# Performance work log

Hardware: AMD Instinct MI355X
Metric: run time of the kernel (lower is better)

## Reference

```python
import jax, jax.numpy as jnp
import numpy as np

HEADS = 16
DIM_HEAD = 64

def setup_inputs() -> dict:
    key = jax.random.key(0)
    ks = jax.random.split(key, 7)
    B, Nq, Dq = 4, 2048, 1024
    Nk, Dc = 1024, 768
    inner = HEADS * DIM_HEAD  # 1024
    sq = 1.0 / np.sqrt(Dq)
    sc = 1.0 / np.sqrt(Dc)
    si = 1.0 / np.sqrt(inner)
    return {
        "x": jax.random.normal(ks[0], (B, Nq, Dq), dtype=jnp.float32),
        "context": jax.random.normal(ks[1], (B, Nk, Dc), dtype=jnp.float32),
        "Wq": jax.random.normal(ks[2], (Dq, inner), dtype=jnp.float32) * sq,
        "Wk": jax.random.normal(ks[3], (Dc, inner), dtype=jnp.float32) * sc,
        "Wv": jax.random.normal(ks[4], (Dc, inner), dtype=jnp.float32) * sc,
        "Wo": jax.random.normal(ks[5], (inner, Dq), dtype=jnp.float32) * si,
        "bo": jax.random.normal(ks[6], (Dq,), dtype=jnp.float32) * 0.01,
    }

def reference(x, context, Wq, Wk, Wv, Wo, bo):
    B, Nq, _ = x.shape
    Nk = context.shape[1]
    h, dh = HEADS, DIM_HEAD
    # projections (no bias on q/k/v, matching nn.Linear(bias=False))
    q = (x @ Wq).reshape(B, Nq, h, dh)        # [B,Nq,h,dh]
    k = (context @ Wk).reshape(B, Nk, h, dh)  # [B,Nk,h,dh]
    v = (context @ Wv).reshape(B, Nk, h, dh)
    scale = 1.0 / jnp.sqrt(jnp.asarray(dh, dtype=x.dtype))
    # scores: [B,h,Nq,Nk]
    scores = jnp.einsum('bqhd,bkhd->bhqk', q, k) * scale
    attn = jax.nn.softmax(scores, axis=-1)
    out = jnp.einsum('bhqk,bkhd->bqhd', attn, v).reshape(B, Nq, h * dh)
    return out @ Wo + bo
```

## Files before the change

kernel.cpp:

```cpp
#include <hip/hip_runtime.h>

typedef __bf16 bf16;
typedef __bf16 bf16x2 __attribute__((ext_vector_type(2)));
typedef __bf16 bf16x4 __attribute__((ext_vector_type(4)));
typedef __bf16 bf16x8 __attribute__((ext_vector_type(8)));
typedef float f32x4 __attribute__((ext_vector_type(4)));

#define MFMA(a, b, c) __builtin_amdgcn_mfma_f32_16x16x32_bf16(a, b, c, 0, 0, 0)

#define GLD16(gptr, ldsptr)                                                        \
  __builtin_amdgcn_global_load_lds(                                                \
      (const __attribute__((address_space(1))) unsigned int*)(gptr),               \
      (__attribute__((address_space(3))) unsigned int*)(ldsptr), 16, 0, 0)

union I4B8 { int4 i; bf16x8 v; };
union HI { bf16x2 h; int i; };

__global__ __launch_bounds__(256) void prep_k(const float* __restrict__ x, bf16* __restrict__ xb,
                                              const float* __restrict__ ctx, bf16* __restrict__ ctxb,
                                              const float* __restrict__ Wq, bf16* __restrict__ WqT,
                                              const float* __restrict__ Wk, bf16* __restrict__ WkvT,
                                              const float* __restrict__ Wv,
                                              const float* __restrict__ Wo, bf16* __restrict__ WoT) {
  __shared__ float t[32][33];
  const int bid = blockIdx.x;
  if (bid < 5632) {
    const float* in; bf16* out; size_t i;
    if (bid < 4096) { in = x; out = xb; i = ((size_t)bid * 256 + threadIdx.x) * 8; }
    else { in = ctx; out = ctxb; i = ((size_t)(bid - 4096) * 256 + threadIdx.x) * 8; }
    const float4 a = *(const float4*)(in + i);
    const float4 b = *(const float4*)(in + i + 4);
    bf16x8 o;
    o[0] = (bf16)a.x; o[1] = (bf16)a.y; o[2] = (bf16)a.z; o[3] = (bf16)a.w;
    o[4] = (bf16)b.x; o[5] = (bf16)b.y; o[6] = (bf16)b.z; o[7] = (bf16)b.w;
    *(bf16x8*)(out + i) = o;
    return;
  }
  const int tt = bid - 5632;
  const int z = tt >> 10, rem = tt & 1023;
  const float* in; bf16* out; int R; float sc = 1.0f;
  if (z == 0)      { in = Wq; out = WqT;                R = 1024; sc = 0.18033688f; }
  else if (z == 1) { in = Wk; out = WkvT;               R = 768; }
  else if (z == 2) { in = Wv; out = WkvT + 1024 * 768;  R = 768; }
  else             { in = Wo; out = WoT;                R = 1024; }
  const int c0 = (rem & 31) * 32, r0 = (rem >> 5) * 32;
  if (r0 >= R) return;
  const int tx = threadIdx.x & 31, ty = threadIdx.x >> 5;
#pragma unroll
  for (int i = 0; i < 4; i++)
    t[ty + i * 8][tx] = in[(size_t)(r0 + ty + i * 8) * 1024 + c0 + tx];
  __syncthreads();
#pragma unroll
  for (int i = 0; i < 4; i++)
    out[(size_t)(c0 + ty + i * 8) * R + r0 + tx] = (bf16)(t[tx][ty + i * 8] * sc);
}

template <int MODE>
__device__ __forceinline__ void gemm_body(const bf16* __restrict__ A,
                                          const bf16* __restrict__ Bt,
                                          int K, int m0, int n0,
                                          void* __restrict__ C0,
                                          const float* __restrict__ bias,
                                          bf16* As, bf16* Bs) {
  const int tid = threadIdx.x;
  const int lane = tid & 63, wave = tid >> 6;
  const int wm = wave >> 1, wn = wave & 1;
  const int q = lane >> 4, c = lane & 15;

  f32x4 acc[4][4] = {};
  const int r = tid >> 3;
  const int col8 = ((tid & 7) * 8) ^ ((r & 7) * 8);
  const bf16* Ag = A + (size_t)(m0 + r) * K + col8;
  const bf16* Bg = Bt + (size_t)(n0 + r) * K + col8;
  const size_t K32 = (size_t)K * 32;
  bf16* AsW = As + wave * 512;
  bf16* BsW = Bs + wave * 512;
  const int swz = (c & 7) * 8;

  for (int k0 = 0; k0 < K; k0 += 64) {
    __syncthreads();
    GLD16(Ag + k0,            AsW);
    GLD16(Ag + k0 + K32,      AsW + 2048);
    GLD16(Ag + k0 + 2 * K32,  AsW + 4096);
    GLD16(Ag + k0 + 3 * K32,  AsW + 6144);
    GLD16(Bg + k0,            BsW);
    GLD16(Bg + k0 + K32,      BsW + 2048);
    GLD16(Bg + k0 + 2 * K32,  BsW + 4096);
    GLD16(Bg + k0 + 3 * K32,  BsW + 6144);
    __syncthreads();
#pragma unroll
    for (int kk = 0; kk < 2; kk++) {
      const int cx = (kk * 32 + q * 8) ^ swz;
      bf16x8 af[4], bfr[4];
#pragma unroll
      for (int mi = 0; mi < 4; mi++)
        af[mi] = *(const bf16x8*)&As[(wm * 64 + mi * 16 + c) * 64 + cx];
#pragma unroll
      for (int ni = 0; ni < 4; ni++)
        bfr[ni] = *(const bf16x8*)&Bs[(wn * 64 + ni * 16 + c) * 64 + cx];
      __builtin_amdgcn_s_setprio(1);
#pragma unroll
      for (int mi = 0; mi < 4; mi++)
#pragma unroll
        for (int ni = 0; ni < 4; ni++) {
          if constexpr (MODE == 2)
            acc[mi][ni] = MFMA(af[mi], bfr[ni], acc[mi][ni]);
          else
            acc[mi][ni] = MFMA(bfr[ni], af[mi], acc[mi][ni]);
        }
      __builtin_amdgcn_s_setprio(0);
    }
  }

  if constexpr (MODE == 0 || MODE == 1) {
#pragma unroll
    for (int ni = 0; ni < 4; ni++) {
      const int col = n0 + wn * 64 + ni * 16 + q * 4;
      float4 bv4 = {};
      if constexpr (MODE == 1) bv4 = *(const float4*)&bias[col];
#pragma unroll
      for (int mi = 0; mi < 4; mi++) {
        const int row = m0 + wm * 64 + mi * 16 + c;
        if constexpr (MODE == 0) {
          bf16x4 vv;
#pragma unroll
          for (int r2 = 0; r2 < 4; r2++) vv[r2] = (bf16)acc[mi][ni][r2];
          *(bf16x4*)&((bf16*)C0)[(size_t)row * 1024 + col] = vv;
        } else {
          f32x4 vv;
          vv[0] = acc[mi][ni][0] + bv4.x; vv[1] = acc[mi][ni][1] + bv4.y;
          vv[2] = acc[mi][ni][2] + bv4.z; vv[3] = acc[mi][ni][3] + bv4.w;
          *(f32x4*)&((float*)C0)[(size_t)row * 1024 + col] = vv;
        }
      }
    }
  } else {
#pragma unroll
    for (int ni = 0; ni < 4; ni++) {
      const int col = n0 + wn * 64 + ni * 16 + c;
#pragma unroll
      for (int mi = 0; mi < 4; mi++) {
        const int rbase = m0 + wm * 64 + mi * 16 + q * 4;
        const int b = rbase >> 10, key = rbase & 1023;
        bf16* VT = (bf16*)C0;
        const int h = col >> 6, d = col & 63;
        const int kl = key & 63;
        const int pkey = (key & ~63) | (kl & 32) | ((kl & 12) << 1) | ((kl & 16) >> 2);
        bf16x4 vv;
#pragma unroll
        for (int r2 = 0; r2 < 4; r2++) vv[r2] = (bf16)acc[mi][ni][r2];
        *(bf16x4*)&VT[((size_t)(b * 16 + h) * 64 + d) * 1024 + pkey] = vv;
      }
    }
  }
}

__global__ __launch_bounds__(256) void proj_k(const bf16* __restrict__ xb,
                                              const bf16* __restrict__ ctxb,
                                              const bf16* __restrict__ WqT,
                                              const bf16* __restrict__ WkvT,
                                              bf16* __restrict__ Q,
                                              bf16* __restrict__ Kp,
                                              bf16* __restrict__ VT) {
  __shared__ __align__(16) bf16 As[8192];
  __shared__ __align__(16) bf16 Bs[8192];
  const int bid = blockIdx.x;
  if (bid < 512) {
    const int s = (bid & 7) * 64 + (bid >> 3);
    gemm_body<0>(xb, WqT, 1024, (s >> 3) * 128, (s & 7) * 128, Q, nullptr, As, Bs);
  } else if (bid < 768) {
    const int t = bid - 512;
    const int s = (t & 7) * 32 + (t >> 3);
    gemm_body<0>(ctxb, WkvT, 768, (s >> 3) * 128, (s & 7) * 128, Kp, nullptr, As, Bs);
  } else {
    const int t = bid - 768;
    const int s = (t & 7) * 32 + (t >> 3);
    gemm_body<2>(ctxb, WkvT + (size_t)1024 * 768, 768, (s >> 3) * 128, (s & 7) * 128,
                 VT, nullptr, As, Bs);
  }
}

__global__ __launch_bounds__(256) void out_k(const bf16* __restrict__ O,
                                             const bf16* __restrict__ WoT,
                                             float* __restrict__ out,
                                             const float* __restrict__ bo) {
  __shared__ __align__(16) bf16 As[8192];
  __shared__ __align__(16) bf16 Bs[8192];
  const int bid = blockIdx.x;
  const int s = (bid & 7) * 64 + (bid >> 3);
  gemm_body<1>(O, WoT, 1024, (s >> 3) * 128, (s & 7) * 128, out, bo, As, Bs);
}

__global__ __launch_bounds__(256, 2) void attn_k(const bf16* __restrict__ Qg,
                                                 const bf16* __restrict__ Kg,
                                                 const bf16* __restrict__ VTg,
                                                 bf16* __restrict__ Og) {
  __shared__ __align__(16) bf16 Ks[64][72];
  __shared__ __align__(16) bf16 Vt[64][72];
  const int tid = threadIdx.x;
  const int lane = tid & 63, w = tid >> 6;
  const int q = lane >> 4, c = lane & 15;
  const int bid = blockIdx.x;
  const int pair = (bid & 7) * 8 + (bid >> 6);
  const int head = pair & 15, b = pair >> 4;
  const int q0 = ((bid >> 3) & 7) * 256;

  bf16x8 aQ[4][2];
#pragma unroll
  for (int mj = 0; mj < 4; mj++)
#pragma unroll
    for (int ks = 0; ks < 2; ks++)
      aQ[mj][ks] = *(const bf16x8*)(Qg + (size_t)(b * 2048 + q0 + w * 64 + mj * 16 + c) * 1024 +
                                    head * 64 + ks * 32 + q * 8);

  f32x4 o[4][4] = {};
  f32x4 ol[4] = {};
  bf16x8 vone;
#pragma unroll
  for (int i = 0; i < 8; i++) vone[i] = (bf16)1.0f;

  const int srow = tid >> 2, sc = tid & 3;
  const bf16* Kbase = Kg + (size_t)(b * 1024 + srow) * 1024 + head * 64 + sc * 16;
  const bf16* Vbase = VTg + ((size_t)(b * 16 + head) * 64 + srow) * 1024 + sc * 16;

  bf16x8 rk0 = *(const bf16x8*)(Kbase);
  bf16x8 rk1 = *(const bf16x8*)(Kbase + 8);
  bf16x8 rv0 = *(const bf16x8*)(Vbase);
  bf16x8 rv1 = *(const bf16x8*)(Vbase + 8);

  for (int kt = 0; kt < 16; kt++) {
    __syncthreads();
    *(bf16x8*)&Ks[srow][sc * 16]     = rk0;
    *(bf16x8*)&Ks[srow][sc * 16 + 8] = rk1;
    *(bf16x8*)&Vt[srow][sc * 16]     = rv0;
    *(bf16x8*)&Vt[srow][sc * 16 + 8] = rv1;
    if (kt < 15) {
      const size_t ko = (size_t)(kt + 1) * 64 * 1024;
      const int vo = (kt + 1) * 64;
      rk0 = *(const bf16x8*)(Kbase + ko);
      rk1 = *(const bf16x8*)(Kbase + ko + 8);
      rv0 = *(const bf16x8*)(Vbase + vo);
      rv1 = *(const bf16x8*)(Vbase + vo + 8);
    }
    __syncthreads();

    f32x4 st[4][4] = {};
#pragma unroll
    for (int ks = 0; ks < 2; ks++) {
      bf16x8 ak[4];
#pragma unroll
      for (int ni = 0; ni < 4; ni++) ak[ni] = *(const bf16x8*)&Ks[ni * 16 + c][ks * 32 + q * 8];
      __builtin_amdgcn_s_setprio(1);
#pragma unroll
      for (int mj = 0; mj < 4; mj++)
#pragma unroll
        for (int ni = 0; ni < 4; ni++)
          st[mj][ni] = MFMA(ak[ni], aQ[mj][ks], st[mj][ni]);
      __builtin_amdgcn_s_setprio(0);
    }

    int pk[4][4][2];
#pragma unroll
    for (int mj = 0; mj < 4; mj++)
#pragma unroll
      for (int ni = 0; ni < 4; ni++) {
        float p0 = __builtin_amdgcn_exp2f(st[mj][ni][0]);
        float p1 = __builtin_amdgcn_exp2f(st[mj][ni][1]);
        float p2 = __builtin_amdgcn_exp2f(st[mj][ni][2]);
        float p3 = __builtin_amdgcn_exp2f(st[mj][ni][3]);
        HI h0, h1;
        h0.h[0] = (bf16)p0; h0.h[1] = (bf16)p1;
        h1.h[0] = (bf16)p2; h1.h[1] = (bf16)p3;
        pk[mj][ni][0] = h0.i;
        pk[mj][ni][1] = h1.i;
      }

#pragma unroll
    for (int ks2 = 0; ks2 < 2; ks2++) {
      bf16x8 bv[4];
#pragma unroll
      for (int ni = 0; ni < 4; ni++)
        bv[ni] = *(const bf16x8*)&Vt[ni * 16 + c][ks2 * 32 + q * 8];
#pragma unroll
      for (int mi = 0; mi < 4; mi++) {
        I4B8 pa;
        pa.i.x = pk[mi][2 * ks2][0];
        pa.i.y = pk[mi][2 * ks2][1];
        pa.i.z = pk[mi][2 * ks2 + 1][0];
        pa.i.w = pk[mi][2 * ks2 + 1][1];
        __builtin_amdgcn_s_setprio(1);
#pragma unroll
        for (int ni = 0; ni < 4; ni++)
          o[mi][ni] = MFMA(pa.v, bv[ni], o[mi][ni]);
        ol[mi] = MFMA(pa.v, vone, ol[mi]);
        __builtin_amdgcn_s_setprio(0);
      }
    }
  }

#pragma unroll
  for (int mi = 0; mi < 4; mi++) {
    float inv[4];
#pragma unroll
    for (int r = 0; r < 4; r++) inv[r] = 1.0f / ol[mi][r];
#pragma unroll
    for (int ni = 0; ni < 4; ni++)
#pragma unroll
      for (int r = 0; r < 4; r++) {
        const int qrow = q0 + w * 64 + mi * 16 + q * 4 + r;
        const int col = head * 64 + ni * 16 + c;
        Og[(size_t)(b * 2048 + qrow) * 1024 + col] = (bf16)(o[mi][ni][r] * inv[r]);
      }
  }
}

extern "C" void kernel_launch(void* const* d_in, const int* in_sizes, int n_in,
                              void* d_out, int out_size, void* d_ws, size_t ws_size,
                              hipStream_t stream) {
  (void)in_sizes; (void)n_in; (void)out_size; (void)ws_size;
  const float* x   = (const float*)d_in[0];
  const float* ctx = (const float*)d_in[1];
  const float* Wq  = (const float*)d_in[2];
  const float* Wk  = (const float*)d_in[3];
  const float* Wv  = (const float*)d_in[4];
  const float* Wo  = (const float*)d_in[5];
  const float* bo  = (const float*)d_in[6];
  float* out = (float*)d_out;

  char* ws = (char*)d_ws;
  const size_t MB = 1u << 20;
  bf16* WqT  = (bf16*)(ws);
  bf16* WkvT = (bf16*)(ws + 2 * MB);
  bf16* WoT  = (bf16*)(ws + 5 * MB);
  bf16* ctxb = (bf16*)(ws + 7 * MB);
  bf16* xb   = (bf16*)(ws + 13 * MB);
  bf16* Q    = (bf16*)(ws + 29 * MB);
  bf16* Kp   = (bf16*)(ws + 45 * MB);
  bf16* VT   = (bf16*)(ws + 53 * MB);
  bf16* O    = xb;

  prep_k<<<5632 + 4096, 256, 0, stream>>>(x, xb, ctx, ctxb, Wq, WqT, Wk, WkvT, Wv, Wo, WoT);

  proj_k<<<1024, 256, 0, stream>>>(xb, ctxb, WqT, WkvT, Q, Kp, VT);

  attn_k<<<512, 256, 0, stream>>>(Q, Kp, VT, O);

  out_k<<<512, 256, 0, stream>>>(O, WoT, out, bo);
}
```

Measured before the change: 205.1 us.

## Use 256x256 double-buffered 8-wave GEMM tiles for QKV projection

Replaces the 128x128 projection GEMM with a 256x256 tile, 512-thread kernel that double-buffers 64-wide K slabs in 128KB of dynamic LDS. Loads for the next slab are interleaved across four quadrant MMA phases with explicit vmcnt waits and barriers. The goal is higher arithmetic intensity per byte loaded and overlap of global-to-LDS copies with MFMA work. In exchange, only 256 blocks run with one block per CU, so load balance and occupancy depend on the hand-written wait scheduling.

Measured after the change: 206.3 us. About the same (+0.5%).

```diff
diff --git a/kernel.cpp b/kernel.cpp
--- a/kernel.cpp
+++ b/kernel.cpp
@@ -56,6 +56,168 @@
 }
 
 template <int MODE>
+__device__ __forceinline__ void phase_mma(const bf16* Ls, int Abase, int Bbase,
+                                          int wm, int wn, int q, int c, int swz,
+                                          f32x4 (&pacc)[4][2]) {
+  bf16x8 af[4][2], bb[2][2];
+#pragma unroll
+  for (int mi = 0; mi < 4; mi++) {
+    const int rr = wm * 64 + mi * 16 + c;
+#pragma unroll
+    for (int kk = 0; kk < 2; kk++)
+      af[mi][kk] = *(const bf16x8*)&Ls[Abase + rr * 64 + ((kk * 32 + q * 8) ^ swz)];
+  }
+#pragma unroll
+  for (int ni = 0; ni < 2; ni++) {
+    const int rn = wn * 32 + ni * 16 + c;
+#pragma unroll
+    for (int kk = 0; kk < 2; kk++)
+      bb[ni][kk] = *(const bf16x8*)&Ls[Bbase + rn * 64 + ((kk * 32 + q * 8) ^ swz)];
+  }
+  __builtin_amdgcn_s_setprio(1);
+#pragma unroll
+  for (int mi = 0; mi < 4; mi++)
+#pragma unroll
+    for (int ni = 0; ni < 2; ni++)
+#pragma unroll
+      for (int kk = 0; kk < 2; kk++) {
+        if constexpr (MODE == 2)
+          pacc[mi][ni] = MFMA(af[mi][kk], bb[ni][kk], pacc[mi][ni]);
+        else
+          pacc[mi][ni] = MFMA(bb[ni][kk], af[mi][kk], pacc[mi][ni]);
+      }
+  __builtin_amdgcn_s_setprio(0);
+}
+
+template <int MODE>
+__device__ __forceinline__ void gemm256(const bf16* __restrict__ A,
+                                        const bf16* __restrict__ Bt,
+                                        int K, int m0, int n0,
+                                        void* __restrict__ C0,
+                                        bf16* Ls) {
+  const int tid = threadIdx.x;
+  const int lane = tid & 63, w = tid >> 6;
+  const int wm = w >> 2, wn = w & 3;
+  const int q = lane >> 4, c = lane & 15;
+  const int swz = (c & 7) * 8;
+
+  const int rl = tid >> 3, seg = tid & 7;
+  const bf16* Ag = A + (size_t)(m0 + rl) * K + ((seg ^ (rl & 7)) * 8);
+  const bf16* Bg = Bt + (size_t)(n0 + rl) * K + ((seg ^ (rl & 7)) * 8);
+  const size_t K64 = (size_t)K * 64, K128 = (size_t)K * 128;
+  const int ws = w * 512;
+
+  f32x4 acc[2][2][4][2] = {};
+
+  GLD16(Ag,              &Ls[0 + ws]);
+  GLD16(Ag + K64,        &Ls[4096 + ws]);
+  GLD16(Ag + K128,       &Ls[8192 + ws]);
+  GLD16(Ag + K128 + K64, &Ls[8192 + 4096 + ws]);
+  GLD16(Bg,              &Ls[32768 + ws]);
+  GLD16(Bg + K64,        &Ls[32768 + 4096 + ws]);
+  GLD16(Bg + K128,       &Ls[32768 + 8192 + ws]);
+  GLD16(Bg + K128 + K64, &Ls[32768 + 8192 + 4096 + ws]);
+
+  int cur = 0;
+  for (int k0 = 0; k0 < K; k0 += 64) {
+    const int nxt = cur ^ 1;
+    const size_t kn = (size_t)((k0 + 64 < K) ? k0 + 64 : k0);
+    const int Ab = cur * 16384, Bb = 32768 + cur * 16384;
+    const int An = nxt * 16384, Bn = 32768 + nxt * 16384;
+
+    asm volatile("s_waitcnt vmcnt(2)" ::: "memory");
+    asm volatile("s_barrier" ::: "memory");
+    GLD16(Ag + kn,       &Ls[An + ws]);
+    GLD16(Ag + kn + K64, &Ls[An + 4096 + ws]);
+    phase_mma<MODE>(Ls, Ab, Bb, wm, wn, q, c, swz, acc[0][0]);
+
+    asm volatile("s_waitcnt vmcnt(2)" ::: "memory");
+    asm volatile("s_barrier" ::: "memory");
+    GLD16(Ag + kn + K128,       &Ls[An + 8192 + ws]);
+    GLD16(Ag + kn + K128 + K64, &Ls[An + 8192 + 4096 + ws]);
+    phase_mma<MODE>(Ls, Ab, Bb + 8192, wm, wn, q, c, swz, acc[0][1]);
+
+    asm volatile("s_barrier" ::: "memory");
+    GLD16(Bg + kn,       &Ls[Bn + ws]);
+    GLD16(Bg + kn + K64, &Ls[Bn + 4096 + ws]);
+    phase_mma<MODE>(Ls, Ab + 8192, Bb, wm, wn, q, c, swz, acc[1][0]);
+
+    asm volatile("s_barrier" ::: "memory");
+    GLD16(Bg + kn + K128,       &Ls[Bn + 8192 + ws]);
+    GLD16(Bg + kn + K128 + K64, &Ls[Bn + 8192 + 4096 + ws]);
+    phase_mma<MODE>(Ls, Ab + 8192, Bb + 8192, wm, wn, q, c, swz, acc[1][1]);
+
+    cur = nxt;
+  }
+  asm volatile("s_waitcnt vmcnt(0)" ::: "memory");
+
+  if constexpr (MODE == 0) {
+#pragma unroll
+    for (int h = 0; h < 2; h++)
+#pragma unroll
+      for (int g = 0; g < 2; g++)
+#pragma unroll
+        for (int ni = 0; ni < 2; ni++) {
+          const int col = n0 + g * 128 + wn * 32 + ni * 16 + q * 4;
+#pragma unroll
+          for (int mi = 0; mi < 4; mi++) {
+            const int row = m0 + h * 128 + wm * 64 + mi * 16 + c;
+            bf16x4 vv;
+#pragma unroll
+            for (int r2 = 0; r2 < 4; r2++) vv[r2] = (bf16)acc[h][g][mi][ni][r2];
+            *(bf16x4*)&((bf16*)C0)[(size_t)row * 1024 + col] = vv;
+          }
+        }
+  } else {
+#pragma unroll
+    for (int h = 0; h < 2; h++)
+#pragma unroll
+      for (int g = 0; g < 2; g++)
+#pragma unroll
+        for (int ni = 0; ni < 2; ni++) {
+          const int col = n0 + g * 128 + wn * 32 + ni * 16 + c;
+#pragma unroll
+          for (int mi = 0; mi < 4; mi++) {
+            const int rbase = m0 + h * 128 + wm * 64 + mi * 16 + q * 4;
+            const int b = rbase >> 10, key = rbase & 1023;
+            bf16* VT = (bf16*)C0;
+            const int hh = col >> 6, d = col & 63;
+            const int kl = key & 63;
+            const int pkey = (key & ~63) | (kl & 32) | ((kl & 12) << 1) | ((kl & 16) >> 2);
+            bf16x4 vv;
+#pragma unroll
+            for (int r2 = 0; r2 < 4; r2++) vv[r2] = (bf16)acc[h][g][mi][ni][r2];
+            *(bf16x4*)&VT[((size_t)(b * 16 + hh) * 64 + d) * 1024 + pkey] = vv;
+          }
+        }
+  }
+}
+
+__global__ __launch_bounds__(512) void proj_k(const bf16* __restrict__ xb,
+                                              const bf16* __restrict__ ctxb,
+                                              const bf16* __restrict__ WqT,
+                                              const bf16* __restrict__ WkvT,
+                                              bf16* __restrict__ Q,
+                                              bf16* __restrict__ Kp,
+                                              bf16* __restrict__ VT) {
+  extern __shared__ __align__(16) bf16 Ls[];
+  const int bid = blockIdx.x;
+  if (bid < 128) {
+    const int x = bid & 7, i = bid >> 3;
+    const int rt = x * 4 + (i >> 2), ct = i & 3;
+    gemm256<0>(xb, WqT, 1024, rt * 256, ct * 256, Q, Ls);
+  } else if (bid < 192) {
+    const int t = bid - 128, x = t & 7, i = t >> 3;
+    const int rt = x * 2 + (i >> 2), ct = i & 3;
+    gemm256<0>(ctxb, WkvT, 768, rt * 256, ct * 256, Kp, Ls);
+  } else {
+    const int t = bid - 192, x = t & 7, i = t >> 3;
+    const int rt = x * 2 + (i >> 2), ct = i & 3;
+    gemm256<2>(ctxb, WkvT + (size_t)1024 * 768, 768, rt * 256, ct * 256, VT, Ls);
+  }
+}
+
+template <int MODE>
 __device__ __forceinline__ void gemm_body(const bf16* __restrict__ A,
                                           const bf16* __restrict__ Bt,
                                           int K, int m0, int n0,
@@ -102,81 +264,24 @@
 #pragma unroll
       for (int mi = 0; mi < 4; mi++)
 #pragma unroll
-        for (int ni = 0; ni < 4; ni++) {
-          if constexpr (MODE == 2)
-            acc[mi][ni] = MFMA(af[mi], bfr[ni], acc[mi][ni]);
-          else
-            acc[mi][ni] = MFMA(bfr[ni], af[mi], acc[mi][ni]);
-        }
+        for (int ni = 0; ni < 4; ni++)
+          acc[mi][ni] = MFMA(bfr[ni], af[mi], acc[mi][ni]);
       __builtin_amdgcn_s_setprio(0);
     }
   }
 
-  if constexpr (MODE == 0 || MODE == 1) {
-#pragma unroll
-    for (int ni = 0; ni < 4; ni++) {
-      const int col = n0 + wn * 64 + ni * 16 + q * 4;
-      float4 bv4 = {};
-      if constexpr (MODE == 1) bv4 = *(const float4*)&bias[col];
-#pragma unroll
-      for (int mi = 0; mi < 4; mi++) {
-        const int row = m0 + wm * 64 + mi * 16 + c;
-        if constexpr (MODE == 0) {
-          bf16x4 vv;
-#pragma unroll
-          for (int r2 = 0; r2 < 4; r2++) vv[r2] = (bf16)acc[mi][ni][r2];
-          *(bf16x4*)&((bf16*)C0)[(size_t)row * 1024 + col] = vv;
-        } else {
-          f32x4 vv;
-          vv[0] = acc[mi][ni][0] + bv4.x; vv[1] = acc[mi][ni][1] + bv4.y;
-          vv[2] = acc[mi][ni][2] + bv4.z; vv[3] = acc[mi][ni][3] + bv4.w;
-          *(f32x4*)&((float*)C0)[(size_t)row * 1024 + col] = vv;
-        }
-      }
+#pragma unroll
+  for (int ni = 0; ni < 4; ni++) {
+    const int col = n0 + wn * 64 + ni * 16 + q * 4;
+    float4 bv4 = *(const float4*)&bias[col];
+#pragma unroll
+    for (int mi = 0; mi < 4; mi++) {
+      const int row = m0 + wm * 64 + mi * 16 + c;
+      f32x4 vv;
+      vv[0] = acc[mi][ni][0] + bv4.x; vv[1] = acc[mi][ni][1] + bv4.y;
+      vv[2] = acc[mi][ni][2] + bv4.z; vv[3] = acc[mi][ni][3] + bv4.w;
+      *(f32x4*)&((float*)C0)[(size_t)row * 1024 + col] = vv;
     }
-  } else {
-#pragma unroll
-    for (int ni = 0; ni < 4; ni++) {
-      const int col = n0 + wn * 64 + ni * 16 + c;
-#pragma unroll
-      for (int mi = 0; mi < 4; mi++) {
-        const int rbase = m0 + wm * 64 + mi * 16 + q * 4;
-        const int b = rbase >> 10, key = rbase & 1023;
-        bf16* VT = (bf16*)C0;
-        const int h = col >> 6, d = col & 63;
-        const int kl = key & 63;
-        const int pkey = (key & ~63) | (kl & 32) | ((kl & 12) << 1) | ((kl & 16) >> 2);
-        bf16x4 vv;
-#pragma unroll
-        for (int r2 = 0; r2 < 4; r2++) vv[r2] = (bf16)acc[mi][ni][r2];
-        *(bf16x4*)&VT[((size_t)(b * 16 + h) * 64 + d) * 1024 + pkey] = vv;
-      }
-    }
-  }
-}
-
-__global__ __launch_bounds__(256) void proj_k(const bf16* __restrict__ xb,
-                                              const bf16* __restrict__ ctxb,
-                                              const bf16* __restrict__ WqT,
-                                              const bf16* __restrict__ WkvT,
-                                              bf16* __restrict__ Q,
-                                              bf16* __restrict__ Kp,
-                                              bf16* __restrict__ VT) {
-  __shared__ __align__(16) bf16 As[8192];
-  __shared__ __align__(16) bf16 Bs[8192];
-  const int bid = blockIdx.x;
-  if (bid < 512) {
-    const int s = (bid & 7) * 64 + (bid >> 3);
-    gemm_body<0>(xb, WqT, 1024, (s >> 3) * 128, (s & 7) * 128, Q, nullptr, As, Bs);
-  } else if (bid < 768) {
-    const int t = bid - 512;
-    const int s = (t & 7) * 32 + (t >> 3);
-    gemm_body<0>(ctxb, WkvT, 768, (s >> 3) * 128, (s & 7) * 128, Kp, nullptr, As, Bs);
-  } else {
-    const int t = bid - 768;
-    const int s = (t & 7) * 32 + (t >> 3);
-    gemm_body<2>(ctxb, WkvT + (size_t)1024 * 768, 768, (s >> 3) * 128, (s & 7) * 128,
-                 VT, nullptr, As, Bs);
   }
 }
 
@@ -341,7 +446,7 @@
 
   prep_k<<<5632 + 4096, 256, 0, stream>>>(x, xb, ctx, ctxb, Wq, WqT, Wk, WkvT, Wv, Wo, WoT);
 
-  proj_k<<<1024, 256, 0, stream>>>(xb, ctxb, WqT, WkvT, Q, Kp, VT);
+  proj_k<<<256, 512, 131072, stream>>>(xb, ctxb, WqT, WkvT, Q, Kp, VT);
 
   attn_k<<<512, 256, 0, stream>>>(Q, Kp, VT, O);
 
```
